# Performance work log

Hardware: AMD Instinct MI355X
Metric: run time of the kernel (lower is better)

## Reference

```python
import jax, jax.numpy as jnp
import numpy as np
from jax import lax

B, C, H, W = 8, 32, 256, 512
MAXDISP = 48


def setup_inputs() -> dict:
    key = jax.random.key(0)
    k1, k2 = jax.random.split(key)
    x = jax.random.normal(k1, (B, C, H, W), dtype=jnp.float32)
    y = jax.random.normal(k2, (B, C, H, W), dtype=jnp.float32)
    return {"x": x, "y": y, "maxdisp": MAXDISP}


def reference(x, y, maxdisp):
    # cost[:, d, :, w] = mean_c( x[:, :, :, w] * y[:, :, :, w-d] ) for w >= d, else 0
    width = x.shape[-1]
    col = jnp.arange(width)

    def step(_, d):
        # roll y right by d along width; wrapped columns are masked out below
        y_shift = jnp.roll(y, d, axis=-1)              # [B,C,H,W]
        c = jnp.mean(x * y_shift, axis=1)              # [B,H,W]
        c = jnp.where(col >= d, c, jnp.float32(0))     # zero invalid (wrapped) cols
        return None, c

    _, cost = lax.scan(step, None, jnp.arange(maxdisp))  # [D,B,H,W]
    return jnp.transpose(cost, (1, 0, 2, 3))             # [B,D,H,W]
```

## Files before the change

kernel.cpp:

```cpp
#include <hip/hip_runtime.h>


constexpr int kB = 8;
constexpr int kC = 32;
constexpr int kH = 256;
constexpr int kW = 512;
constexpr int kD = 48;

constexpr int WT = 128;
constexpr int YW = kD + WT;
constexpr int NT = 128;
constexpr int CH = 16;
constexpr int DP = 12;
constexpr int WP = 4;

__global__ __launch_bounds__(NT) void corr_kernel(
    const float* __restrict__ x, const float* __restrict__ y, float* __restrict__ out)
{
    __shared__ __align__(16) float xs[CH][WT];
    __shared__ __align__(16) float ys[CH][YW];

    const int tid = threadIdx.x;
    const int w0  = blockIdx.x * WT;
    const int h   = blockIdx.y;
    const int b   = blockIdx.z;

    const size_t cs = (size_t)kH * kW;
    const float* xb = x + ((size_t)b * kC * kH + h) * kW + w0;
    const float* yb = y + ((size_t)b * kC * kH + h) * kW + (w0 - kD);

    const int lw    = tid & 31;
    const int dgrp  = tid >> 5;
    const int wi    = lw << 2;
    const int d0    = dgrp * DP;
    const int ybase = wi + 36 - d0;

    float acc[DP][WP];
    #pragma unroll
    for (int dd = 0; dd < DP; ++dd)
        #pragma unroll
        for (int j = 0; j < WP; ++j) acc[dd][j] = 0.f;

    for (int p = 0; p < 2; ++p) {
        if (p) __syncthreads();

        #pragma unroll
        for (int idx = tid; idx < CH * (WT / 4); idx += NT) {
            int c   = idx >> 5;
            int col = (idx & 31) << 2;
            *(float4*)&xs[c][col] =
                *(const float4*)(xb + (size_t)(p * CH + c) * cs + col);
        }
        #pragma unroll
        for (int idx = tid; idx < CH * (YW / 4); idx += NT) {
            int c   = idx / (YW / 4);
            int col = (idx % (YW / 4)) << 2;
            float4 v = make_float4(0.f, 0.f, 0.f, 0.f);
            if (w0 - kD + col >= 0)
                v = *(const float4*)(yb + (size_t)(p * CH + c) * cs + col);
            *(float4*)&ys[c][col] = v;
        }
        __syncthreads();

        #pragma unroll 4
        for (int c = 0; c < CH; ++c) {
            float4 x4 = *(const float4*)&xs[c][wi];
            float4 y0 = *(const float4*)&ys[c][ybase];
            float4 y1 = *(const float4*)&ys[c][ybase + 4];
            float4 y2 = *(const float4*)&ys[c][ybase + 8];
            float4 y3 = *(const float4*)&ys[c][ybase + 12];
            float xv[4]  = {x4.x, x4.y, x4.z, x4.w};
            float yv[16] = {y0.x, y0.y, y0.z, y0.w, y1.x, y1.y, y1.z, y1.w,
                            y2.x, y2.y, y2.z, y2.w, y3.x, y3.y, y3.z, y3.w};
            #pragma unroll
            for (int dd = 0; dd < DP; ++dd)
                #pragma unroll
                for (int j = 0; j < WP; ++j)
                    acc[dd][j] += xv[j] * yv[j + 12 - dd];
        }
    }

    const float scale = 1.0f / kC;
    #pragma unroll
    for (int dd = 0; dd < DP; ++dd) {
        float* o = out + (((size_t)b * kD + d0 + dd) * kH + h) * kW + w0 + wi;
        *(float4*)o = make_float4(acc[dd][0] * scale, acc[dd][1] * scale,
                                  acc[dd][2] * scale, acc[dd][3] * scale);
    }
}

extern "C" void kernel_launch(void* const* d_in, const int* in_sizes, int n_in,
                              void* d_out, int out_size, void* d_ws, size_t ws_size,
                              hipStream_t stream) {
    const float* x = (const float*)d_in[0];
    const float* y = (const float*)d_in[1];
    float* out = (float*)d_out;

    dim3 grid(kW / WT, kH, kB);
    corr_kernel<<<grid, NT, 0, stream>>>(x, y, out);
}
```

Before: 410.5 us.

## Load y tile via direct global-to-LDS DMA, read x from global, use six disparity groups

The y tile is staged into shared memory with global_load_lds DMA, so data no longer passes through registers. The left-edge zero padding is now written after the load with an extra barrier. The x tile is no longer staged; each thread reads its float4 of x straight from global memory. The block grows to 192 threads with 8 disparities per thread instead of 12, which lowers register pressure and raises occupancy (launch bounds 6). The cost is more redundant global reads of x across the disparity groups and a sync for the edge blocks.

Measured after the change: 401.5 us. 2.2% less time.

```diff
diff --git a/kernel.cpp b/kernel.cpp
--- a/kernel.cpp
+++ b/kernel.cpp
@@ -9,16 +9,22 @@
 
 constexpr int WT = 128;
 constexpr int YW = kD + WT;
-constexpr int NT = 128;
+constexpr int NT = 192;
 constexpr int CH = 16;
-constexpr int DP = 12;
+constexpr int DP = 8;
 constexpr int WP = 4;
+constexpr int NCHUNK = CH * YW * 4 / 1024;
 
-__global__ __launch_bounds__(NT) void corr_kernel(
+__device__ __forceinline__ void load_lds16(const float* g, float* l) {
+    __builtin_amdgcn_global_load_lds(
+        (const __attribute__((address_space(1))) void*)g,
+        (__attribute__((address_space(3))) void*)l, 16, 0, 0);
+}
+
+__global__ __launch_bounds__(NT, 6) void corr_kernel(
     const float* __restrict__ x, const float* __restrict__ y, float* __restrict__ out)
 {
-    __shared__ __align__(16) float xs[CH][WT];
-    __shared__ __align__(16) float ys[CH][YW];
+    __shared__ __align__(16) float ys[CH * YW];
 
     const int tid = threadIdx.x;
     const int w0  = blockIdx.x * WT;
@@ -26,14 +32,18 @@
     const int b   = blockIdx.z;
 
     const size_t cs = (size_t)kH * kW;
-    const float* xb = x + ((size_t)b * kC * kH + h) * kW + w0;
-    const float* yb = y + ((size_t)b * kC * kH + h) * kW + (w0 - kD);
 
     const int lw    = tid & 31;
     const int dgrp  = tid >> 5;
     const int wi    = lw << 2;
     const int d0    = dgrp * DP;
-    const int ybase = wi + 36 - d0;
+    const int ybase = wi + 40 - d0;
+
+    const int wv = tid >> 6;
+    const int ln = tid & 63;
+
+    const float* xbh = x + ((size_t)b * kC * kH + h) * kW + w0 + wi;
+    const float* ybh = y + ((size_t)b * kC * kH + h) * kW;
 
     float acc[DP][WP];
     #pragma unroll
@@ -44,39 +54,39 @@
     for (int p = 0; p < 2; ++p) {
         if (p) __syncthreads();
 
-        #pragma unroll
-        for (int idx = tid; idx < CH * (WT / 4); idx += NT) {
-            int c   = idx >> 5;
-            int col = (idx & 31) << 2;
-            *(float4*)&xs[c][col] =
-                *(const float4*)(xb + (size_t)(p * CH + c) * cs + col);
-        }
-        #pragma unroll
-        for (int idx = tid; idx < CH * (YW / 4); idx += NT) {
-            int c   = idx / (YW / 4);
-            int col = (idx % (YW / 4)) << 2;
-            float4 v = make_float4(0.f, 0.f, 0.f, 0.f);
-            if (w0 - kD + col >= 0)
-                v = *(const float4*)(yb + (size_t)(p * CH + c) * cs + col);
-            *(float4*)&ys[c][col] = v;
+        for (int k = wv; k < NCHUNK; k += 3) {
+            const int f   = (k << 8) + (ln << 2);
+            const int r   = f / YW;
+            const int col = f - r * YW;
+            int wcol = w0 - kD + col;
+            if (wcol < 0) wcol = 0;
+            load_lds16(ybh + (size_t)(p * CH + r) * cs + wcol, &ys[k << 8]);
         }
         __syncthreads();
 
-        #pragma unroll 4
+        if (w0 == 0) {
+            for (int idx = tid; idx < CH * kD; idx += NT) {
+                const int r = idx / kD;
+                ys[r * YW + (idx - r * kD)] = 0.f;
+            }
+            __syncthreads();
+        }
+
+        #pragma unroll 2
         for (int c = 0; c < CH; ++c) {
-            float4 x4 = *(const float4*)&xs[c][wi];
-            float4 y0 = *(const float4*)&ys[c][ybase];
-            float4 y1 = *(const float4*)&ys[c][ybase + 4];
-            float4 y2 = *(const float4*)&ys[c][ybase + 8];
-            float4 y3 = *(const float4*)&ys[c][ybase + 12];
-            float xv[4]  = {x4.x, x4.y, x4.z, x4.w};
-            float yv[16] = {y0.x, y0.y, y0.z, y0.w, y1.x, y1.y, y1.z, y1.w,
-                            y2.x, y2.y, y2.z, y2.w, y3.x, y3.y, y3.z, y3.w};
+            const float4 x4 = *(const float4*)(xbh + (size_t)(p * CH + c) * cs);
+            const float* yc = &ys[c * YW + ybase];
+            const float4 y0 = *(const float4*)(yc);
+            const float4 y1 = *(const float4*)(yc + 4);
+            const float4 y2 = *(const float4*)(yc + 8);
+            const float xv[4]  = {x4.x, x4.y, x4.z, x4.w};
+            const float yv[12] = {y0.x, y0.y, y0.z, y0.w, y1.x, y1.y, y1.z, y1.w,
+                                  y2.x, y2.y, y2.z, y2.w};
             #pragma unroll
             for (int dd = 0; dd < DP; ++dd)
                 #pragma unroll
                 for (int j = 0; j < WP; ++j)
-                    acc[dd][j] += xv[j] * yv[j + 12 - dd];
+                    acc[dd][j] += xv[j] * yv[8 + j - dd];
         }
     }
 
```
